# Performance work log

Hardware: AMD Instinct MI355X
Metric: run time of the kernel (lower is better)

Reference implementation:

```python
import jax, jax.numpy as jnp
import numpy as np

EPS = 1e-10   # eps added inside cumprod, as in _compute_weights
FAR = 1e10    # last delta, as in forward()
NEAR_D, FAR_D = 2.0, 6.0  # typical NeRF near/far bounds for depth sampling

N_RAYS, N_PTS = 65536, 128


def setup_inputs() -> dict:
    key = jax.random.key(0)
    k1, k2, k3 = jax.random.split(key, 3)
    # densities are non-negative (raw sigma output after relu/softplus)
    density = jax.random.uniform(k1, (N_RAYS, N_PTS), dtype=jnp.float32) * 2.0
    feature = jax.random.uniform(k2, (N_RAYS, N_PTS, 3), dtype=jnp.float32)
    # monotonically increasing sample depths along each ray in [NEAR_D, FAR_D]
    depth_values = jnp.sort(
        jax.random.uniform(k3, (N_RAYS, N_PTS), dtype=jnp.float32,
                           minval=NEAR_D, maxval=FAR_D), axis=-1)
    return {"density": density, "feature": feature, "depth_values": depth_values}


def reference(density, feature, depth_values):
    # deltas: diff of sample depths, last delta = 1e10  -> [N, P]
    deltas = jnp.concatenate(
        [depth_values[..., 1:] - depth_values[..., :-1],
         jnp.full_like(depth_values[..., :1], FAR)], axis=-1)
    alpha = 1.0 - jnp.exp(-deltas * density)                      # [N, P]
    # transmittance: cumprod(1-alpha+eps) rolled right with T[...,0]=1
    Tinc = jnp.cumprod(1.0 - alpha + EPS, axis=-1)                # [N, P]
    T = jnp.concatenate([jnp.ones_like(Tinc[..., :1]), Tinc[..., :-1]], axis=-1)
    weights = T * alpha                                           # [N, P]
    # weighted feature (rgb) and depth aggregation over samples
    rgb = jnp.einsum('np,npc->nc', weights, feature)              # [N, 3]
    depth = jnp.einsum('np,npc->nc', weights,
                       jnp.broadcast_to(depth_values[..., None], feature.shape))  # [N, 3]
    return rgb, depth
```

## Files before the change

kernel.cpp:

```cpp
#include <hip/hip_runtime.h>

#define N_PTS 128
#define EPS_F 1e-10f
#define FAR_F 1e10f
#define RAYS_PER_BLOCK 8
#define MAX_GRID 2048

template<int CTRL, int ROW_MASK>
__device__ __forceinline__ float dpp_mov(float src, float old) {
    union { float f; int i; } s, o, r;
    s.f = src; o.f = old;
    r.i = __builtin_amdgcn_update_dpp(o.i, s.i, CTRL, ROW_MASK, 0xF, false);
    return r.f;
}

__device__ __forceinline__ float half32_reduce_add(float x) {
    x += dpp_mov<0x111, 0xF>(x, 0.0f);
    x += dpp_mov<0x112, 0xF>(x, 0.0f);
    x += dpp_mov<0x114, 0xF>(x, 0.0f);
    x += dpp_mov<0x118, 0xF>(x, 0.0f);
    x += dpp_mov<0x142, 0xA>(x, 0.0f);
    return x;
}

__global__ __launch_bounds__(256) void volrend_kernel(
        const float* __restrict__ density,
        const float* __restrict__ feature,
        const float* __restrict__ depth,
        float* __restrict__ out, int n_rays, int iters) {
    const int lane = threadIdx.x & 63;
    const int sub  = lane & 31;
    const int h    = lane >> 5;
    const int wid  = threadIdx.x >> 6;
    const int stride8 = gridDim.x * RAYS_PER_BLOCK;

    __shared__ float sbuf[2][64];

    int base8 = blockIdx.x * RAYS_PER_BLOCK;

    {
        const int ray = base8 + (wid << 1) + h;
        const size_t dz = (size_t)ray * N_PTS + (sub << 2);
    }
    int ray0 = base8 + (wid << 1) + h;
    size_t dz0 = (size_t)ray0 * N_PTS + (sub << 2);
    float4 dns = *(const float4*)(density + dz0);
    float4 zz  = *(const float4*)(depth   + dz0);
    const float4* fp0 = (const float4*)(feature + (size_t)ray0 * (N_PTS * 3) + sub * 12);
    float4 fa = fp0[0], fb = fp0[1], fc = fp0[2];

    for (int it = 0; it < iters; ++it) {
        const bool more = (it + 1) < iters;
        float4 ndns, nzz, nfa, nfb, nfc;
        if (more) {
            const int nray = base8 + stride8 + (wid << 1) + h;
            const size_t ndz = (size_t)nray * N_PTS + (sub << 2);
            ndns = *(const float4*)(density + ndz);
            nzz  = *(const float4*)(depth   + ndz);
            const float4* nfp = (const float4*)(feature + (size_t)nray * (N_PTS * 3) + sub * 12);
            nfa = nfp[0]; nfb = nfp[1]; nfc = nfp[2];
        }

        float nz = dpp_mov<0x130, 0xF>(zz.x, 0.0f);
        float d0 = zz.y - zz.x;
        float d1 = zz.z - zz.y;
        float d2 = zz.w - zz.z;
        float d3 = (sub == 31) ? FAR_F : (nz - zz.w);

        float e0 = __expf(-d0 * dns.x);
        float e1 = __expf(-d1 * dns.y);
        float e2 = __expf(-d2 * dns.z);
        float e3 = __expf(-d3 * dns.w);
        float a0 = 1.0f - e0, a1 = 1.0f - e1, a2 = 1.0f - e2, a3 = 1.0f - e3;
        float f0 = e0 + EPS_F, f1 = e1 + EPS_F, f2 = e2 + EPS_F, f3 = e3 + EPS_F;

        float f01  = f0 * f1;
        float f012 = f01 * f2;
        float p    = f012 * f3;
        p *= dpp_mov<0x111, 0xF>(p, 1.0f);
        p *= dpp_mov<0x112, 0xF>(p, 1.0f);
        p *= dpp_mov<0x114, 0xF>(p, 1.0f);
        p *= dpp_mov<0x118, 0xF>(p, 1.0f);
        p *= dpp_mov<0x142, 0xA>(p, 1.0f);
        float Ts = dpp_mov<0x138, 0xF>(p, 1.0f);
        if (sub == 0) Ts = 1.0f;

        float w0 = Ts   * a0;
        float T1 = Ts   * f0;   float w1 = T1 * a1;
        float T2 = Ts   * f01;  float w2 = T2 * a2;
        float T3 = Ts   * f012; float w3 = T3 * a3;

        float rx = half32_reduce_add(w0 * fa.x + w1 * fa.w + w2 * fb.z + w3 * fc.y);
        float ry = half32_reduce_add(w0 * fa.y + w1 * fb.x + w2 * fb.w + w3 * fc.z);
        float rz = half32_reduce_add(w0 * fa.z + w1 * fb.y + w2 * fc.x + w3 * fc.w);
        float dd = half32_reduce_add(w0 * zz.x + w1 * zz.y + w2 * zz.z + w3 * zz.w);

        const int b = it & 1;
        if (sub == 31) {
            const int r8 = (wid << 1) + h;
            sbuf[b][r8 * 3 + 0] = rx;
            sbuf[b][r8 * 3 + 1] = ry;
            sbuf[b][r8 * 3 + 2] = rz;
            sbuf[b][32 + r8 * 3 + 0] = dd;
            sbuf[b][32 + r8 * 3 + 1] = dd;
            sbuf[b][32 + r8 * 3 + 2] = dd;
        }
        __syncthreads();
        {
            const int t = threadIdx.x;
            float* orgb = out + (size_t)base8 * 3;
            float* odep = out + (size_t)n_rays * 3 + (size_t)base8 * 3;
            if (t < 24)                     orgb[t]      = sbuf[b][t];
            else if (t >= 32 && t < 56)     odep[t - 32] = sbuf[b][t];
        }

        if (more) { dns = ndns; zz = nzz; fa = nfa; fb = nfb; fc = nfc; }
        base8 += stride8;
    }
}

extern "C" void kernel_launch(void* const* d_in, const int* in_sizes, int n_in,
                              void* d_out, int out_size, void* d_ws, size_t ws_size,
                              hipStream_t stream) {
    const float* density = (const float*)d_in[0];
    const float* feature = (const float*)d_in[1];
    const float* depth   = (const float*)d_in[2];
    float* out = (float*)d_out;
    const int n_rays = in_sizes[0] / N_PTS;
    int nblk8 = n_rays / RAYS_PER_BLOCK;
    int grid = nblk8 < MAX_GRID ? nblk8 : MAX_GRID;
    while (grid > 1 && (nblk8 % grid)) --grid;
    const int iters = nblk8 / grid;
    volrend_kernel<<<grid, 256, 0, stream>>>(density, feature, depth, out,
                                             n_rays, iters);
}
```

Baseline: 193.7 us.

## Double-buffer ray loads two iterations ahead and drop block-level shared-memory sync

Restructures the grid-stride loop so each wave keeps two register buffers of ray data in flight, issuing loads two iterations ahead instead of one. It also removes the shared-memory staging and __syncthreads per iteration, having lane 31 of each half-wave write its outputs directly to global memory. The aim is more memory-level parallelism and no block-wide barriers, at the cost of higher register pressure and scattered small global stores instead of coalesced ones.

```diff
diff --git a/kernel.cpp b/kernel.cpp
--- a/kernel.cpp
+++ b/kernel.cpp
@@ -3,7 +3,6 @@
 #define N_PTS 128
 #define EPS_F 1e-10f
 #define FAR_F 1e10f
-#define RAYS_PER_BLOCK 8
 #define MAX_GRID 2048
 
 template<int CTRL, int ROW_MASK>
@@ -23,6 +22,52 @@
     return x;
 }
 
+__device__ __forceinline__ void process_pair(
+        const float4& dns, const float4& zz,
+        const float4& fa, const float4& fb, const float4& fc,
+        int sub, int ray, int n_rays, float* __restrict__ out) {
+    float nz = dpp_mov<0x130, 0xF>(zz.x, 0.0f);
+    float d0 = zz.y - zz.x;
+    float d1 = zz.z - zz.y;
+    float d2 = zz.w - zz.z;
+    float d3 = (sub == 31) ? FAR_F : (nz - zz.w);
+
+    float e0 = __expf(-d0 * dns.x);
+    float e1 = __expf(-d1 * dns.y);
+    float e2 = __expf(-d2 * dns.z);
+    float e3 = __expf(-d3 * dns.w);
+    float a0 = 1.0f - e0, a1 = 1.0f - e1, a2 = 1.0f - e2, a3 = 1.0f - e3;
+    float f0 = e0 + EPS_F, f1 = e1 + EPS_F, f2 = e2 + EPS_F, f3 = e3 + EPS_F;
+
+    float f01  = f0 * f1;
+    float f012 = f01 * f2;
+    float p    = f012 * f3;
+    p *= dpp_mov<0x111, 0xF>(p, 1.0f);
+    p *= dpp_mov<0x112, 0xF>(p, 1.0f);
+    p *= dpp_mov<0x114, 0xF>(p, 1.0f);
+    p *= dpp_mov<0x118, 0xF>(p, 1.0f);
+    p *= dpp_mov<0x142, 0xA>(p, 1.0f);
+    float Ts = dpp_mov<0x138, 0xF>(p, 1.0f);
+    if (sub == 0) Ts = 1.0f;
+
+    float w0 = Ts * a0;
+    float T1 = Ts * f0;   float w1 = T1 * a1;
+    float T2 = Ts * f01;  float w2 = T2 * a2;
+    float T3 = Ts * f012; float w3 = T3 * a3;
+
+    float rx = half32_reduce_add(w0 * fa.x + w1 * fa.w + w2 * fb.z + w3 * fc.y);
+    float ry = half32_reduce_add(w0 * fa.y + w1 * fb.x + w2 * fb.w + w3 * fc.z);
+    float rz = half32_reduce_add(w0 * fa.z + w1 * fb.y + w2 * fc.x + w3 * fc.w);
+    float dd = half32_reduce_add(w0 * zz.x + w1 * zz.y + w2 * zz.z + w3 * zz.w);
+
+    if (sub == 31) {
+        float* o  = out + (size_t)ray * 3;
+        o[0] = rx; o[1] = ry; o[2] = rz;
+        float* od = out + (size_t)n_rays * 3 + (size_t)ray * 3;
+        od[0] = dd; od[1] = dd; od[2] = dd;
+    }
+}
+
 __global__ __launch_bounds__(256) void volrend_kernel(
         const float* __restrict__ density,
         const float* __restrict__ feature,
@@ -31,91 +76,51 @@
     const int lane = threadIdx.x & 63;
     const int sub  = lane & 31;
     const int h    = lane >> 5;
-    const int wid  = threadIdx.x >> 6;
-    const int stride8 = gridDim.x * RAYS_PER_BLOCK;
+    const int gw   = blockIdx.x * 4 + (threadIdx.x >> 6);
+    const int rstep = gridDim.x * 4 * 2;
 
-    __shared__ float sbuf[2][64];
+    int ray0 = gw * 2 + h;
+    size_t doff = (size_t)ray0 * N_PTS + (sub << 2);
+    size_t foff = (size_t)ray0 * (N_PTS * 3) + sub * 12;
+    const size_t dstep = (size_t)rstep * N_PTS;
+    const size_t fstep = (size_t)rstep * (N_PTS * 3);
 
-    int base8 = blockIdx.x * RAYS_PER_BLOCK;
+    float4 dA = *(const float4*)(density + doff);
+    float4 zA = *(const float4*)(depth   + doff);
+    const float4* fpA = (const float4*)(feature + foff);
+    float4 aA = fpA[0], bA = fpA[1], cA = fpA[2];
 
-    {
-        const int ray = base8 + (wid << 1) + h;
-        const size_t dz = (size_t)ray * N_PTS + (sub << 2);
+    float4 dB, zB, aB, bB, cB;
+    if (iters > 1) {
+        dB = *(const float4*)(density + doff + dstep);
+        zB = *(const float4*)(depth   + doff + dstep);
+        const float4* fpB = (const float4*)(feature + foff + fstep);
+        aB = fpB[0]; bB = fpB[1]; cB = fpB[2];
     }
-    int ray0 = base8 + (wid << 1) + h;
-    size_t dz0 = (size_t)ray0 * N_PTS + (sub << 2);
-    float4 dns = *(const float4*)(density + dz0);
-    float4 zz  = *(const float4*)(depth   + dz0);
-    const float4* fp0 = (const float4*)(feature + (size_t)ray0 * (N_PTS * 3) + sub * 12);
-    float4 fa = fp0[0], fb = fp0[1], fc = fp0[2];
+    doff += 2 * dstep; foff += 2 * fstep;
 
-    for (int it = 0; it < iters; ++it) {
-        const bool more = (it + 1) < iters;
-        float4 ndns, nzz, nfa, nfb, nfc;
-        if (more) {
-            const int nray = base8 + stride8 + (wid << 1) + h;
-            const size_t ndz = (size_t)nray * N_PTS + (sub << 2);
-            ndns = *(const float4*)(density + ndz);
-            nzz  = *(const float4*)(depth   + ndz);
-            const float4* nfp = (const float4*)(feature + (size_t)nray * (N_PTS * 3) + sub * 12);
-            nfa = nfp[0]; nfb = nfp[1]; nfc = nfp[2];
+    int ray_c = ray0;
+    for (int k = 0; k < iters; k += 2) {
+        process_pair(dA, zA, aA, bA, cA, sub, ray_c, n_rays, out);
+        if (k + 2 < iters) {
+            dA = *(const float4*)(density + doff);
+            zA = *(const float4*)(depth   + doff);
+            const float4* fp = (const float4*)(feature + foff);
+            aA = fp[0]; bA = fp[1]; cA = fp[2];
+            doff += dstep; foff += fstep;
         }
+        ray_c += rstep;
+        if (k + 1 >= iters) break;
 
-        float nz = dpp_mov<0x130, 0xF>(zz.x, 0.0f);
-        float d0 = zz.y - zz.x;
-        float d1 = zz.z - zz.y;
-        float d2 = zz.w - zz.z;
-        float d3 = (sub == 31) ? FAR_F : (nz - zz.w);
-
-        float e0 = __expf(-d0 * dns.x);
-        float e1 = __expf(-d1 * dns.y);
-        float e2 = __expf(-d2 * dns.z);
-        float e3 = __expf(-d3 * dns.w);
-        float a0 = 1.0f - e0, a1 = 1.0f - e1, a2 = 1.0f - e2, a3 = 1.0f - e3;
-        float f0 = e0 + EPS_F, f1 = e1 + EPS_F, f2 = e2 + EPS_F, f3 = e3 + EPS_F;
-
-        float f01  = f0 * f1;
-        float f012 = f01 * f2;
-        float p    = f012 * f3;
-        p *= dpp_mov<0x111, 0xF>(p, 1.0f);
-        p *= dpp_mov<0x112, 0xF>(p, 1.0f);
-        p *= dpp_mov<0x114, 0xF>(p, 1.0f);
-        p *= dpp_mov<0x118, 0xF>(p, 1.0f);
-        p *= dpp_mov<0x142, 0xA>(p, 1.0f);
-        float Ts = dpp_mov<0x138, 0xF>(p, 1.0f);
-        if (sub == 0) Ts = 1.0f;
-
-        float w0 = Ts   * a0;
-        float T1 = Ts   * f0;   float w1 = T1 * a1;
-        float T2 = Ts   * f01;  float w2 = T2 * a2;
-        float T3 = Ts   * f012; float w3 = T3 * a3;
-
-        float rx = half32_reduce_add(w0 * fa.x + w1 * fa.w + w2 * fb.z + w3 * fc.y);
-        float ry = half32_reduce_add(w0 * fa.y + w1 * fb.x + w2 * fb.w + w3 * fc.z);
-        float rz = half32_reduce_add(w0 * fa.z + w1 * fb.y + w2 * fc.x + w3 * fc.w);
-        float dd = half32_reduce_add(w0 * zz.x + w1 * zz.y + w2 * zz.z + w3 * zz.w);
-
-        const int b = it & 1;
-        if (sub == 31) {
-            const int r8 = (wid << 1) + h;
-            sbuf[b][r8 * 3 + 0] = rx;
-            sbuf[b][r8 * 3 + 1] = ry;
-            sbuf[b][r8 * 3 + 2] = rz;
-            sbuf[b][32 + r8 * 3 + 0] = dd;
-            sbuf[b][32 + r8 * 3 + 1] = dd;
-            sbuf[b][32 + r8 * 3 + 2] = dd;
+        process_pair(dB, zB, aB, bB, cB, sub, ray_c, n_rays, out);
+        if (k + 3 < iters) {
+            dB = *(const float4*)(density + doff);
+            zB = *(const float4*)(depth   + doff);
+            const float4* fp = (const float4*)(feature + foff);
+            aB = fp[0]; bB = fp[1]; cB = fp[2];
+            doff += dstep; foff += fstep;
         }
-        __syncthreads();
-        {
-            const int t = threadIdx.x;
-            float* orgb = out + (size_t)base8 * 3;
-            float* odep = out + (size_t)n_rays * 3 + (size_t)base8 * 3;
-            if (t < 24)                     orgb[t]      = sbuf[b][t];
-            else if (t >= 32 && t < 56)     odep[t - 32] = sbuf[b][t];
-        }
-
-        if (more) { dns = ndns; zz = nzz; fa = nfa; fb = nfb; fc = nfc; }
-        base8 += stride8;
+        ray_c += rstep;
     }
 }
 
@@ -127,7 +132,7 @@
     const float* depth   = (const float*)d_in[2];
     float* out = (float*)d_out;
     const int n_rays = in_sizes[0] / N_PTS;
-    int nblk8 = n_rays / RAYS_PER_BLOCK;
+    int nblk8 = n_rays / 8;
     int grid = nblk8 < MAX_GRID ? nblk8 : MAX_GRID;
     while (grid > 1 && (nblk8 % grid)) --grid;
     const int iters = nblk8 / grid;
```

New measurement: 192.4 us. About the same (-0.7%).
